# Performance work log

Measured on AMD Instinct MI355X. Metric: run time of the kernel, lower is better.

The kernel has to match this reference:

```python
import jax, jax.numpy as jnp
import numpy as np

K = 3          # kernel_size
EPS = 1e-12    # epsilon from l2_normal and abs-clamp


def setup_inputs() -> dict:
    key = jax.random.key(0)
    k1, k2 = jax.random.split(key)
    B, H, W, C, F = 8, 224, 224, 32, 32
    image = jax.random.normal(k1, (B, H, W, C), dtype=jnp.float32)
    # glorot-uniform-ish weight, shape (1, C*K*K, filters)
    fan = C * K * K + F
    lim = np.sqrt(6.0 / fan).astype(np.float32)
    w = jax.random.uniform(k2, (1, C * K * K, F), dtype=jnp.float32, minval=-lim, maxval=lim)
    p = jnp.full((F,), 100.0 ** 0.5, dtype=jnp.float32)   # p init = sqrt(100)
    q = jnp.full((1,), 10.0 ** 0.5, dtype=jnp.float32)    # q init = sqrt(10)
    return {"image": image, "w": w, "p": p, "q": q}


def reference(image, w, p, q):
    # CosSim2D, kernel_size=3, stride=1, padding='same', non-depthwise.
    B, H, W, C = image.shape
    pad = K // 2
    padded = jnp.pad(image, ((0, 0), (pad, pad), (pad, pad), (0, 0)))
    # im2col: kernel-position-major, channel-minor -> matches tf.stack(axis=3) + reshape
    patches = jnp.stack(
        [padded[:, dy:dy + H, dx:dx + W, :] for dy in range(K) for dx in range(K)],
        axis=3,
    )  # (B, H, W, K*K, C)
    x = patches.reshape(B, H * W, K * K * C)
    q_term = jnp.square(q) / 10.0                       # scalar (broadcast)
    x_norm = jnp.sqrt(jnp.maximum(jnp.sum(x * x, axis=2, keepdims=True), EPS)) + q_term
    w_norm = jnp.sqrt(jnp.maximum(jnp.sum(w * w, axis=1, keepdims=True), EPS)) + q_term
    sim = jnp.matmul(x / x_norm, (w / w_norm)[0])       # (B, H*W, filters)
    out = jnp.sign(sim) * jnp.power(jnp.abs(sim) + EPS, jnp.square(p) / 100.0)
    return out.reshape(B, H, W, -1)
```

## Files before the change

kernel.cpp:

```cpp
#include <hip/hip_runtime.h>
#include <hip/hip_bf16.h>


#define H_ 224
#define W_ 224
#define C_ 32
#define F_ 32

#define NSTEP 18
#define HROWS 10
#define HCOLS 34
#define NPIX (HROWS * HCOLS)
#define HGRAN (NPIX * 4)
#define HPAD 1536

typedef __bf16 bf16_t;
typedef bf16_t bf16x8 __attribute__((ext_vector_type(8)));
typedef float f32x16 __attribute__((ext_vector_type(16)));

#define WFRAG_BYTES (NSTEP * 64 * 8 * 2)

__device__ __forceinline__ void dma16(const void* gp, void* lp) {
  __builtin_amdgcn_global_load_lds(
      (const __attribute__((address_space(1))) void*)gp,
      (__attribute__((address_space(3))) void*)lp, 16, 0, 0);
}

__global__ __launch_bounds__(256) void cos2d_prep(
    const float* __restrict__ w, const float* __restrict__ p,
    const float* __restrict__ q, bf16_t* __restrict__ wfrag,
    float* __restrict__ winv, float* __restrict__ ef,
    float* __restrict__ zpool) {
  const int tid = threadIdx.x;
  if (blockIdx.x == 0) {
    __shared__ float part[8][32];
    const int f = tid & 31, kg = tid >> 5;
    float s = 0.f;
#pragma unroll
    for (int i = 0; i < 36; ++i) {
      const float v = w[(kg + 8 * i) * F_ + f];
      s += v * v;
    }
    part[kg][f] = s;
    zpool[tid] = 0.f;
    __syncthreads();
    if (tid < 32) {
      float t = 0.f;
#pragma unroll
      for (int g = 0; g < 8; ++g) t += part[g][tid];
      const float qt = q[0] * q[0] * 0.1f;
      winv[tid] = 1.f / (sqrtf(fmaxf(t, 1e-12f)) + qt);
      ef[tid] = p[tid] * p[tid] * 0.01f;
    }
  } else {
    const int t = (blockIdx.x - 1) * 256 + tid;
    if (t < NSTEP * 64) {
      const int s2 = t >> 6, l = t & 63;
      const int ff = l & 31;
      union { bf16_t v[8]; uint4 u; } tv;
#pragma unroll
      for (int e = 0; e < 8; ++e) {
        const int kk = s2 * 16 + ((l >> 5) << 3) + e;
        tv.v[e] = (bf16_t)w[kk * F_ + ff];
      }
      *(uint4*)(wfrag + (size_t)t * 8) = tv.u;
    }
  }
}

__global__ __launch_bounds__(256, 3) void cos2d_main(
    const float* __restrict__ img, const bf16_t* __restrict__ wfrag,
    const float* __restrict__ winv, const float* __restrict__ ef,
    const float* __restrict__ q, const float* __restrict__ zpool,
    float* __restrict__ out) {
  __shared__ __align__(16) float xt[2 * HPAD * 4];

  const int tid = threadIdx.x;
  const int lane = tid & 63;
  const int wv = tid >> 6;
  const int lp = lane & 31;
  const int hi2 = (lane >> 5) * 2;

  const int bid = blockIdx.x;
  const int b  = bid & 7;
  const int tl = bid >> 3;
  const int tw = tl % 7, th = tl / 7;
  const int h0 = th * 8, w0 = tw * 32;

  const float qt = q[0] * q[0] * 0.1f;
  const float efv = ef[lp];
  const float wnv = winv[lp];
  const bool allfast = __all(__builtin_fabsf(efv - 1.0f) < 1e-6f);

  bf16x8 bfrag[NSTEP];
  const bf16x8* wf4 = (const bf16x8*)wfrag;
#pragma unroll
  for (int s2 = 0; s2 < NSTEP; ++s2) bfrag[s2] = wf4[s2 * 64 + lane];

#pragma unroll
  for (int k = 0; k < 12; ++k) {
    const int s = k * 256 + tid;
    const int half = k >= 6;
    const int u = s - half * HPAD;
    float* lb = &xt[(size_t)(k * 256 + wv * 64) * 4];
    const int uc = u < HGRAN ? u : 0;
    const int pp = uc >> 2;
    const int c  = half * 4 + ((uc & 3) ^ ((pp >> 1) & 3));
    const int rr = pp / HCOLS, cc = pp - rr * HCOLS;
    const int hh = h0 - 1 + rr, wc = w0 - 1 + cc;
    const bool live = (u < HGRAN) & ((unsigned)hh < H_) & ((unsigned)wc < W_);
    const float* src = live
        ? img + ((size_t)(b * H_ + hh) * W_ + wc) * C_ + c * 4
        : zpool + lane * 4;
    dma16(src, lb);
  }

  const int mr0 = wv * 2;

  f32x16 acc0, acc1;
#pragma unroll
  for (int i = 0; i < 16; ++i) { acc0[i] = 0.f; acc1[i] = 0.f; }
  float psum[4] = {0.f, 0.f, 0.f, 0.f};

#pragma unroll
  for (int h = 0; h < 2; ++h) {
    if (h == 0) {
      asm volatile("s_waitcnt vmcnt(6)" ::: "memory");
    } else {
      asm volatile("s_waitcnt vmcnt(0)" ::: "memory");
    }
    __builtin_amdgcn_sched_barrier(0);
    __builtin_amdgcn_s_barrier();
    __builtin_amdgcn_sched_barrier(0);

    const int hbase = h * (HPAD * 4);
#pragma unroll
    for (int dx = 0; dx < 3; ++dx) {
      bf16x8 af[4];
#pragma unroll
      for (int r = 0; r < 4; ++r) {
        const int p = (mr0 + r) * HCOLS + lp + dx;
        const int pj = (p >> 1) & 3;
        const int g0 = p * 4 + (hi2 ^ pj);
        const int g1 = p * 4 + ((hi2 + 1) ^ pj);
        const float4 f0 = *(const float4*)&xt[(size_t)(hbase + g0 * 4)];
        const float4 f1 = *(const float4*)&xt[(size_t)(hbase + g1 * 4)];
        psum[r] += f0.x * f0.x + f0.y * f0.y + f0.z * f0.z + f0.w * f0.w +
                   f1.x * f1.x + f1.y * f1.y + f1.z * f1.z + f1.w * f1.w;
        bf16x8 a;
        a[0] = (bf16_t)f0.x; a[1] = (bf16_t)f0.y;
        a[2] = (bf16_t)f0.z; a[3] = (bf16_t)f0.w;
        a[4] = (bf16_t)f1.x; a[5] = (bf16_t)f1.y;
        a[6] = (bf16_t)f1.z; a[7] = (bf16_t)f1.w;
        af[r] = a;
      }
#pragma unroll
      for (int dy = 0; dy < 3; ++dy) {
        const bf16x8 bf = bfrag[2 * (dy * 3 + dx) + h];
        acc0 = __builtin_amdgcn_mfma_f32_32x32x16_bf16(af[dy],     bf, acc0, 0, 0, 0);
        acc1 = __builtin_amdgcn_mfma_f32_32x32x16_bf16(af[dy + 1], bf, acc1, 0, 0, 0);
      }
    }
  }

#pragma unroll
  for (int r = 0; r < 4; ++r) psum[r] += __shfl_xor(psum[r], 32);
  float xinv[2];
  xinv[0] = 1.f / (sqrtf(fmaxf(psum[0] + psum[1] + psum[2], 1e-12f)) + qt);
  xinv[1] = 1.f / (sqrtf(fmaxf(psum[1] + psum[2] + psum[3], 1e-12f)) + qt);

#pragma unroll
  for (int t = 0; t < 2; ++t) {
    const f32x16& acc = t ? acc1 : acc0;
    const int obase = (b * H_ + h0 + mr0 + t) * W_ + w0;
    if (allfast) {
#pragma unroll
      for (int jj = 0; jj < 16; ++jj) {
        const int row = (jj & 3) + 8 * (jj >> 2) + 4 * (lane >> 5);
        const float xi = __shfl(xinv[t], row);
        const float sim = acc[jj] * xi * wnv;
        const float r = copysignf(fabsf(sim) + 1e-12f, sim);
        __builtin_nontemporal_store(r, &out[(size_t)(obase + row) * F_ + lp]);
      }
    } else {
#pragma unroll
      for (int jj = 0; jj < 16; ++jj) {
        const int row = (jj & 3) + 8 * (jj >> 2) + 4 * (lane >> 5);
        const float xi = __shfl(xinv[t], row);
        const float sim = acc[jj] * xi * wnv;
        const float ps = fabsf(sim) + 1e-12f;
        float r = exp2f(efv * __log2f(ps));
        r = copysignf(r, sim);
        __builtin_nontemporal_store(r, &out[(size_t)(obase + row) * F_ + lp]);
      }
    }
  }
}

extern "C" void kernel_launch(void* const* d_in, const int* in_sizes, int n_in,
                              void* d_out, int out_size, void* d_ws, size_t ws_size,
                              hipStream_t stream) {
  const float* img = (const float*)d_in[0];
  const float* w   = (const float*)d_in[1];
  const float* p   = (const float*)d_in[2];
  const float* q   = (const float*)d_in[3];

  bf16_t* wfrag = (bf16_t*)d_ws;
  float*  winv  = (float*)((char*)d_ws + WFRAG_BYTES);
  float*  ef    = winv + 64;
  float*  zpool = ef + 64;

  cos2d_prep<<<6, 256, 0, stream>>>(w, p, q, wfrag, winv, ef, zpool);
  cos2d_main<<<1568, 256, 0, stream>>>(img, wfrag, winv, ef, q, zpool,
                                       (float*)d_out);
}
```

Before: 30.96 us.

## Halve LDS staging buffer and raise occupancy by serializing the channel halves

```diff
diff --git a/kernel.cpp b/kernel.cpp
--- a/kernel.cpp
+++ b/kernel.cpp
@@ -68,12 +68,12 @@
   }
 }
 
-__global__ __launch_bounds__(256, 3) void cos2d_main(
+__global__ __launch_bounds__(256, 4) void cos2d_main(
     const float* __restrict__ img, const bf16_t* __restrict__ wfrag,
     const float* __restrict__ winv, const float* __restrict__ ef,
     const float* __restrict__ q, const float* __restrict__ zpool,
     float* __restrict__ out) {
-  __shared__ __align__(16) float xt[2 * HPAD * 4];
+  __shared__ __align__(16) float xt[HPAD * 4];
 
   const int tid = threadIdx.x;
   const int lane = tid & 63;
@@ -97,23 +97,23 @@
 #pragma unroll
   for (int s2 = 0; s2 < NSTEP; ++s2) bfrag[s2] = wf4[s2 * 64 + lane];
 
-#pragma unroll
-  for (int k = 0; k < 12; ++k) {
-    const int s = k * 256 + tid;
-    const int half = k >= 6;
-    const int u = s - half * HPAD;
-    float* lb = &xt[(size_t)(k * 256 + wv * 64) * 4];
-    const int uc = u < HGRAN ? u : 0;
-    const int pp = uc >> 2;
-    const int c  = half * 4 + ((uc & 3) ^ ((pp >> 1) & 3));
-    const int rr = pp / HCOLS, cc = pp - rr * HCOLS;
-    const int hh = h0 - 1 + rr, wc = w0 - 1 + cc;
-    const bool live = (u < HGRAN) & ((unsigned)hh < H_) & ((unsigned)wc < W_);
-    const float* src = live
-        ? img + ((size_t)(b * H_ + hh) * W_ + wc) * C_ + c * 4
-        : zpool + lane * 4;
-    dma16(src, lb);
-  }
+  auto stage_half = [&](int half) {
+#pragma unroll
+    for (int k = 0; k < 6; ++k) {
+      const int u = k * 256 + tid;
+      float* lb = &xt[(size_t)(k * 256 + wv * 64) * 4];
+      const int uc = u < HGRAN ? u : 0;
+      const int pp = uc >> 2;
+      const int c  = half * 4 + ((uc & 3) ^ ((pp >> 1) & 3));
+      const int rr = pp / HCOLS, cc = pp - rr * HCOLS;
+      const int hh = h0 - 1 + rr, wc = w0 - 1 + cc;
+      const bool live = (u < HGRAN) & ((unsigned)hh < H_) & ((unsigned)wc < W_);
+      const float* src = live
+          ? img + ((size_t)(b * H_ + hh) * W_ + wc) * C_ + c * 4
+          : zpool + lane * 4;
+      dma16(src, lb);
+    }
+  };
 
   const int mr0 = wv * 2;
 
@@ -122,18 +122,7 @@
   for (int i = 0; i < 16; ++i) { acc0[i] = 0.f; acc1[i] = 0.f; }
   float psum[4] = {0.f, 0.f, 0.f, 0.f};
 
-#pragma unroll
-  for (int h = 0; h < 2; ++h) {
-    if (h == 0) {
-      asm volatile("s_waitcnt vmcnt(6)" ::: "memory");
-    } else {
-      asm volatile("s_waitcnt vmcnt(0)" ::: "memory");
-    }
-    __builtin_amdgcn_sched_barrier(0);
-    __builtin_amdgcn_s_barrier();
-    __builtin_amdgcn_sched_barrier(0);
-
-    const int hbase = h * (HPAD * 4);
+  auto compute_half = [&](int h) {
 #pragma unroll
     for (int dx = 0; dx < 3; ++dx) {
       bf16x8 af[4];
@@ -143,8 +132,8 @@
         const int pj = (p >> 1) & 3;
         const int g0 = p * 4 + (hi2 ^ pj);
         const int g1 = p * 4 + ((hi2 + 1) ^ pj);
-        const float4 f0 = *(const float4*)&xt[(size_t)(hbase + g0 * 4)];
-        const float4 f1 = *(const float4*)&xt[(size_t)(hbase + g1 * 4)];
+        const float4 f0 = *(const float4*)&xt[(size_t)g0 * 4];
+        const float4 f1 = *(const float4*)&xt[(size_t)g1 * 4];
         psum[r] += f0.x * f0.x + f0.y * f0.y + f0.z * f0.z + f0.w * f0.w +
                    f1.x * f1.x + f1.y * f1.y + f1.z * f1.z + f1.w * f1.w;
         bf16x8 a;
@@ -161,7 +150,15 @@
         acc1 = __builtin_amdgcn_mfma_f32_32x32x16_bf16(af[dy + 1], bf, acc1, 0, 0, 0);
       }
     }
-  }
+  };
+
+  stage_half(0);
+  __syncthreads();
+  compute_half(0);
+  __syncthreads();
+  stage_half(1);
+  __syncthreads();
+  compute_half(1);
 
 #pragma unroll
   for (int r = 0; r < 4; ++r) psum[r] += __shfl_xor(psum[r], 32);
```

Measured after the change: 95.39 us. 208% more time.
